# Optimization experiments

Hardware: AMD Instinct MI355X
Metric: run time of the kernel (lower is better)

The kernel has to match this reference:

```python
import jax, jax.numpy as jnp
import numpy as np

N = 100000
E = 1600000
F = 128
H = 8
D = F // H
NC = 3


def setup_inputs() -> dict:
    key = jax.random.key(0)
    ks = jax.random.split(key, 12)
    s = lambda fan_in: 1.0 / np.sqrt(fan_in)
    x = jax.random.normal(ks[0], (N, F), dtype=jnp.float32)
    edge_index = jax.random.randint(ks[1], (2, E), 0, N, dtype=jnp.int64)
    edge_attr = jax.random.normal(ks[2], (E, 2), dtype=jnp.float32)
    # params stored as [in, out] so y = x @ W + b
    Wqkv = jax.random.uniform(ks[3], (F, 3 * F), jnp.float32, -s(F), s(F))
    Wedge = jax.random.uniform(ks[4], (2, H), jnp.float32, -s(2), s(2))
    Wout = jax.random.uniform(ks[5], (F, F), jnp.float32, -s(F), s(F))
    bout = jax.random.uniform(ks[6], (F,), jnp.float32, -s(F), s(F))
    ln_w = jnp.ones((F,), jnp.float32)
    ln_b = jnp.zeros((F,), jnp.float32)
    Wc1 = jax.random.uniform(ks[7], (F, F // 2), jnp.float32, -s(F), s(F))
    bc1 = jax.random.uniform(ks[8], (F // 2,), jnp.float32, -s(F), s(F))
    Wc2 = jax.random.uniform(ks[9], (F // 2, NC), jnp.float32, -s(F // 2), s(F // 2))
    bc2 = jax.random.uniform(ks[10], (NC,), jnp.float32, -s(F // 2), s(F // 2))
    return {"x": x, "edge_index": edge_index, "edge_attr": edge_attr,
            "Wqkv": Wqkv, "Wedge": Wedge, "Wout": Wout, "bout": bout,
            "ln_w": ln_w, "ln_b": ln_b,
            "Wc1": Wc1, "bc1": bc1, "Wc2": Wc2, "bc2": bc2}


def reference(x, edge_index, edge_attr, Wqkv, Wedge, Wout, bout,
              ln_w, ln_b, Wc1, bc1, Wc2, bc2):
    n = x.shape[0]
    scale = D ** (-0.5)
    qkv = x @ Wqkv                                # [N, 3F]
    q, k, v = [t.reshape(n, H, D) for t in jnp.split(qkv, 3, axis=-1)]
    src = edge_index[0]   # j (source / neighbor)
    dst = edge_index[1]   # i (target, softmax segment)
    edge_bias = edge_attr @ Wedge                 # [E, H]
    # per-edge biased attention score
    score = jnp.einsum('ehd,ehd->eh', q[dst], k[src]) * scale + edge_bias
    # segment softmax over incoming edges of each target node
    m = jax.lax.stop_gradient(jax.ops.segment_max(score, dst, num_segments=n))
    ex = jnp.exp(score - m[dst])
    denom = jax.ops.segment_sum(ex, dst, num_segments=n) + 1e-16
    w = ex / denom[dst]                           # [E, H]
    agg = jax.ops.segment_sum(v[src] * w[..., None], dst, num_segments=n)
    attn_out = agg.reshape(n, F) @ Wout + bout    # to_out
    h = x + attn_out
    mu = jnp.mean(h, axis=-1, keepdims=True)
    var = jnp.mean((h - mu) ** 2, axis=-1, keepdims=True)
    h = (h - mu) / jnp.sqrt(var + 1e-5) * ln_w + ln_b
    h = jax.nn.relu(h @ Wc1 + bc1)
    return h @ Wc2 + bc2
```

## Files before the change

### kernel.cpp

```cpp
#include <hip/hip_runtime.h>
#include <stdint.h>

#define N_NODES 100000
#define N_EDGES 1600000
#define FDIM 128
#define NH 8
#define NCLS 3
#define NB 782

static constexpr float SCALE = 0.25f;

typedef _Float16 f16x8 __attribute__((ext_vector_type(8)));
typedef _Float16 f16x4 __attribute__((ext_vector_type(4)));
typedef float    f32x4 __attribute__((ext_vector_type(4)));

__global__ __launch_bounds__(256) void k_bhist(const int* __restrict__ ei,
                                               int* __restrict__ bcnt) {
    __shared__ int sb[NB];
    for (int i = threadIdx.x; i < NB; i += 256) sb[i] = 0;
    __syncthreads();
    int e0 = blockIdx.x * 1024;
#pragma unroll
    for (int j = 0; j < 4; ++j) {
        int e = e0 + j * 256 + threadIdx.x;
        if (e < N_EDGES) atomicAdd(&sb[ei[N_EDGES + e] >> 7], 1);
    }
    __syncthreads();
    for (int i = threadIdx.x; i < NB; i += 256)
        if (sb[i]) atomicAdd(&bcnt[i], sb[i]);
}

__global__ __launch_bounds__(256) void k_bscan(const int* __restrict__ bcnt,
                                               int* __restrict__ bbase,
                                               int* __restrict__ bcur) {
    __shared__ int sd[256];
    int t = threadIdx.x;
    int v[4]; int s = 0;
#pragma unroll
    for (int j = 0; j < 4; ++j) {
        int i = t * 4 + j;
        v[j] = (i < NB) ? bcnt[i] : 0;
        s += v[j];
    }
    sd[t] = s;
    __syncthreads();
    for (int off = 1; off < 256; off <<= 1) {
        int a = (t >= off) ? sd[t - off] : 0;
        __syncthreads();
        sd[t] += a;
        __syncthreads();
    }
    int run = sd[t] - s;
#pragma unroll
    for (int j = 0; j < 4; ++j) {
        int i = t * 4 + j;
        if (i < NB) { bbase[i] = run; bcur[i] = run; }
        run += v[j];
    }
    if (t == 0) bbase[NB] = N_EDGES;
}

__global__ __launch_bounds__(256) void k_bin(const int* __restrict__ ei,
                                             const float* __restrict__ ea,
                                             int* __restrict__ bcur,
                                             int* __restrict__ cnt,
                                             float4* __restrict__ binb) {
    __shared__ int lcnt[NB];
    __shared__ int lbase[NB];
    for (int i = threadIdx.x; i < NB; i += 256) lcnt[i] = 0;
    __syncthreads();
    int e0 = blockIdx.x * 1024;
    int rnk[4], bkt[4], src[4], dst[4];
    float2 eav[4];
#pragma unroll
    for (int j = 0; j < 4; ++j) {
        int e = e0 + j * 256 + threadIdx.x;
        if (e < N_EDGES) {
            src[j] = ei[e];
            dst[j] = ei[N_EDGES + e];
            eav[j] = *(const float2*)(ea + (long)e * 2);
            bkt[j] = dst[j] >> 7;
            rnk[j] = atomicAdd(&lcnt[bkt[j]], 1);
            atomicAdd(&cnt[dst[j]], 1);
        } else bkt[j] = -1;
    }
    __syncthreads();
    for (int i = threadIdx.x; i < NB; i += 256)
        if (lcnt[i]) lbase[i] = atomicAdd(&bcur[i], lcnt[i]);
    __syncthreads();
#pragma unroll
    for (int j = 0; j < 4; ++j) {
        if (bkt[j] >= 0) {
            int pos = lbase[bkt[j]] + rnk[j];
            binb[pos] = make_float4(__int_as_float(src[j]), __int_as_float(dst[j]),
                                    eav[j].x, eav[j].y);
        }
    }
}

__global__ __launch_bounds__(256) void k_scan1(const int* __restrict__ cnt,
                                               int* __restrict__ bsum) {
    __shared__ int sd[256];
    int t = threadIdx.x;
    int i0 = blockIdx.x * 1024 + t * 4;
    int s = 0;
#pragma unroll
    for (int j = 0; j < 4; ++j) {
        int i = i0 + j;
        if (i < N_NODES) s += cnt[i];
    }
    sd[t] = s;
    __syncthreads();
    for (int off = 128; off > 0; off >>= 1) {
        if (t < off) sd[t] += sd[t + off];
        __syncthreads();
    }
    if (t == 0) bsum[blockIdx.x] = sd[0];
}

__global__ __launch_bounds__(128) void k_scan2(const int* __restrict__ bsum,
                                               int* __restrict__ boff,
                                               int* __restrict__ row_start) {
    __shared__ int sd[128];
    int t = threadIdx.x;
    int v = (t < 98) ? bsum[t] : 0;
    sd[t] = v;
    __syncthreads();
    for (int off = 1; off < 128; off <<= 1) {
        int add = (t >= off) ? sd[t - off] : 0;
        __syncthreads();
        sd[t] += add;
        __syncthreads();
    }
    if (t < 98) boff[t] = sd[t] - v;
    if (t == 0) row_start[N_NODES] = N_EDGES;
}

__global__ __launch_bounds__(256) void k_scan3(const int* __restrict__ cnt,
                                               const int* __restrict__ boff,
                                               int* __restrict__ row_start) {
    __shared__ int sd[256];
    int t = threadIdx.x;
    int i0 = blockIdx.x * 1024 + t * 4;
    int c[4];
    int s = 0;
#pragma unroll
    for (int j = 0; j < 4; ++j) {
        int i = i0 + j;
        c[j] = (i < N_NODES) ? cnt[i] : 0;
        s += c[j];
    }
    sd[t] = s;
    __syncthreads();
    for (int off = 1; off < 256; off <<= 1) {
        int add = (t >= off) ? sd[t - off] : 0;
        __syncthreads();
        sd[t] += add;
        __syncthreads();
    }
    int run = boff[blockIdx.x] + sd[t] - s;
#pragma unroll
    for (int j = 0; j < 4; ++j) {
        int i = i0 + j;
        if (i < N_NODES) row_start[i] = run;
        run += c[j];
    }
}

__global__ __launch_bounds__(256) void k_fine(const float4* __restrict__ binb,
                                              const int* __restrict__ bbase,
                                              const int* __restrict__ row_start,
                                              float4* __restrict__ se4) {
    __shared__ int cur[128];
    int b = blockIdx.x;
    int n0 = b << 7;
    int t = threadIdx.x;
    if (t < 128) {
        int n = n0 + t;
        cur[t] = (n < N_NODES) ? row_start[n] : 0;
    }
    __syncthreads();
    int p0 = bbase[b], p1 = bbase[b + 1];
    for (int p = p0 + t; p < p1; p += 256) {
        float4 r = binb[p];
        int d = __float_as_int(r.y);
        int pos = atomicAdd(&cur[d - n0], 1);
        se4[pos] = make_float4(r.x, r.z, r.w, 0.f);
    }
}

__global__ __launch_bounds__(256) void k_cvt(const float* __restrict__ x,
                                             const float* __restrict__ Wqkv,
                                             const float* __restrict__ Wout,
                                             _Float16* __restrict__ x_h,
                                             _Float16* __restrict__ Wqkv_t,
                                             _Float16* __restrict__ Wout_t) {
    long i = (long)blockIdx.x * 256 + threadIdx.x;
    float4 v = ((const float4*)x)[i];
    f16x4 h = { (_Float16)v.x, (_Float16)v.y, (_Float16)v.z, (_Float16)v.w };
    *(f16x4*)(x_h + i * 4) = h;
    if (i < 128 * 384) {
        int k = (int)(i / 384), n = (int)(i % 384);
        Wqkv_t[(long)n * 128 + k] = (_Float16)Wqkv[i];
    }
    if (i < 128 * 128) {
        int k = (int)(i / 128), n = (int)(i % 128);
        Wout_t[(long)n * 128 + k] = (_Float16)Wout[i];
    }
}

__global__ __launch_bounds__(256) void k_mm_qkv(const _Float16* __restrict__ x_h,
                                                const _Float16* __restrict__ Wt,
                                                float* __restrict__ q_tab,
                                                _Float16* __restrict__ kv_h) {
    int wave = threadIdx.x >> 6, l = threadIdx.x & 63;
    int row0 = blockIdx.x * 64 + wave * 16;
    int lr = l & 15, lg = l >> 4;
    int arow = row0 + lr;
    bool aok = arow < N_NODES;
    long abase = (long)arow * 128 + lg * 8;

    f32x4 acc[24];
#pragma unroll
    for (int c = 0; c < 24; ++c) acc[c] = (f32x4){0.f, 0.f, 0.f, 0.f};

#pragma unroll
    for (int kk = 0; kk < 4; ++kk) {
        f16x8 a = aok ? *(const f16x8*)(x_h + abase + kk * 32) : (f16x8){};
        const _Float16* wb = Wt + (long)lr * 128 + lg * 8 + kk * 32;
#pragma unroll
        for (int c = 0; c < 24; ++c) {
            f16x8 b = *(const f16x8*)(wb + (long)c * 16 * 128);
            acc[c] = __builtin_amdgcn_mfma_f32_16x16x32_f16(a, b, acc[c], 0, 0, 0);
        }
    }

    int orow_base = row0 + lg * 4;
#pragma unroll
    for (int c = 0; c < 24; ++c) {
#pragma unroll
        for (int j = 0; j < 4; ++j) {
            int orow = orow_base + j;
            if (orow < N_NODES) {
                float v = acc[c][j];
                if (c < 8)       q_tab[(long)orow * 128 + c * 16 + lr] = v;
                else if (c < 16) kv_h[(long)orow * 256 + (c - 8) * 16 + lr]        = (_Float16)v;
                else             kv_h[(long)orow * 256 + 128 + (c - 16) * 16 + lr] = (_Float16)v;
            }
        }
    }
}

__global__ __launch_bounds__(256) void k_mm_out(const _Float16* __restrict__ agg_h,
                                                const _Float16* __restrict__ Wot,
                                                const float* __restrict__ bout,
                                                const float* __restrict__ x,
                                                float* __restrict__ h_pre) {
    int wave = threadIdx.x >> 6, l = threadIdx.x & 63;
    int row0 = blockIdx.x * 64 + wave * 16;
    int lr = l & 15, lg = l >> 4;
    int arow = row0 + lr;
    bool aok = arow < N_NODES;
    long abase = (long)arow * 128 + lg * 8;

    f32x4 acc[8];
#pragma unroll
    for (int c = 0; c < 8; ++c) acc[c] = (f32x4){0.f, 0.f, 0.f, 0.f};

#pragma unroll
    for (int kk = 0; kk < 4; ++kk) {
        f16x8 a = aok ? *(const f16x8*)(agg_h + abase + kk * 32) : (f16x8){};
        const _Float16* wb = Wot + (long)lr * 128 + lg * 8 + kk * 32;
#pragma unroll
        for (int c = 0; c < 8; ++c) {
            f16x8 b = *(const f16x8*)(wb + (long)c * 16 * 128);
            acc[c] = __builtin_amdgcn_mfma_f32_16x16x32_f16(a, b, acc[c], 0, 0, 0);
        }
    }

    int orow_base = row0 + lg * 4;
#pragma unroll
    for (int c = 0; c < 8; ++c) {
        int ocol = c * 16 + lr;
        float bv = bout[ocol];
#pragma unroll
        for (int j = 0; j < 4; ++j) {
            int orow = orow_base + j;
            if (orow < N_NODES) {
                h_pre[(long)orow * 128 + ocol] = acc[c][j] + bv + x[(long)orow * 128 + ocol];
            }
        }
    }
}

__global__ __launch_bounds__(256) void k_attn(const float* __restrict__ q_tab,
                                              const _Float16* __restrict__ kv_tab,
                                              const float4* __restrict__ se4,
                                              const int* __restrict__ row_start,
                                              const float* __restrict__ Wedge,
                                              _Float16* __restrict__ agg_h) {
    int wave = threadIdx.x >> 6;
    int lane = threadIdx.x & 63;
    int node = blockIdx.x * 4 + wave;
    if (node >= N_NODES) return;

    int g  = lane >> 4;
    int gl = lane & 15;
    int h  = gl >> 1;

    int p0 = row_start[node], p1 = row_start[node + 1];
    if (p0 == p1) {
        if (g == 0) *(f16x8*)(agg_h + (long)node * 128 + gl * 8) = (f16x8){};
        return;
    }

    float we0 = Wedge[h];
    float we1 = Wedge[8 + h];
    const float* qb = q_tab + (long)node * 128 + gl * 8;
    float4 qa  = *(const float4*)(qb);
    float4 qbv = *(const float4*)(qb + 4);

    float a0=0.f,a1=0.f,a2=0.f,a3=0.f,a4=0.f,a5=0.f,a6=0.f,a7=0.f;
    float den = 0.f;

    int last = p1 - 1;
    float4 rec = se4[min(p0 + g, last)];
    for (int p = p0; p < p1; p += 4) {
        float4 cur = rec;
        int pn = p + 4;
        if (pn < p1) rec = se4[min(pn + g, last)];

        bool valid = (p + g) < p1;
        int src = __float_as_int(cur.x);
        const _Float16* kvb = kv_tab + (long)src * 256 + gl * 8;
        f16x8 kh = *(const f16x8*)(kvb);
        f16x8 vh = *(const f16x8*)(kvb + 128);

        float part = qa.x  * (float)kh[0] + qa.y  * (float)kh[1]
                   + qa.z  * (float)kh[2] + qa.w  * (float)kh[3]
                   + qbv.x * (float)kh[4] + qbv.y * (float)kh[5]
                   + qbv.z * (float)kh[6] + qbv.w * (float)kh[7];
        part += __shfl_xor(part, 1);

        float s = part * SCALE + cur.y * we0 + cur.z * we1;
        float w = valid ? __expf(s) : 0.f;
        den += w;
        a0 += w * (float)vh[0]; a1 += w * (float)vh[1];
        a2 += w * (float)vh[2]; a3 += w * (float)vh[3];
        a4 += w * (float)vh[4]; a5 += w * (float)vh[5];
        a6 += w * (float)vh[6]; a7 += w * (float)vh[7];
    }

#pragma unroll
    for (int off = 16; off <= 32; off <<= 1) {
        a0 += __shfl_xor(a0, off); a1 += __shfl_xor(a1, off);
        a2 += __shfl_xor(a2, off); a3 += __shfl_xor(a3, off);
        a4 += __shfl_xor(a4, off); a5 += __shfl_xor(a5, off);
        a6 += __shfl_xor(a6, off); a7 += __shfl_xor(a7, off);
        den += __shfl_xor(den, off);
    }

    if (g == 0) {
        float inv = 1.0f / (den + 1e-16f);
        f16x8 o = { (_Float16)(a0 * inv), (_Float16)(a1 * inv),
                    (_Float16)(a2 * inv), (_Float16)(a3 * inv),
                    (_Float16)(a4 * inv), (_Float16)(a5 * inv),
                    (_Float16)(a6 * inv), (_Float16)(a7 * inv) };
        *(f16x8*)(agg_h + (long)node * 128 + gl * 8) = o;
    }
}

__global__ __launch_bounds__(256) void k_mlp(const float* __restrict__ h_pre,
                                             const float* __restrict__ ln_w,
                                             const float* __restrict__ ln_b,
                                             const float* __restrict__ Wc1,
                                             const float* __restrict__ bc1,
                                             const float* __restrict__ Wc2,
                                             const float* __restrict__ bc2,
                                             float* __restrict__ out) {
    __shared__ float sW1[128 * 64];
    __shared__ float sW2[64 * 3];
    __shared__ float sb1[64];
    __shared__ float sb2[3];
    __shared__ float hbuf[4][4][128];
    int t = threadIdx.x;
#pragma unroll
    for (int it = 0; it < 8; ++it) {
        int f = (it * 256 + t) * 4;
        *(float4*)(sW1 + f) = *(const float4*)(Wc1 + f);
    }
    if (t < 192) sW2[t] = Wc2[t];
    if (t < 64) sb1[t] = bc1[t];
    if (t < 3) sb2[t] = bc2[t];
    __syncthreads();

    int wave = t >> 6, lane = t & 63;
    float2 lw = *(const float2*)(ln_w + lane * 2);
    float2 lb = *(const float2*)(ln_b + lane * 2);
    int nb0 = (blockIdx.x * 4 + wave) * 4;

#pragma unroll
    for (int nb = 0; nb < 4; ++nb) {
        int node = nb0 + nb;
        float2 hv = *(const float2*)(h_pre + (long)node * 128 + lane * 2);
        float s = hv.x + hv.y;
#pragma unroll
        for (int off = 32; off > 0; off >>= 1) s += __shfl_xor(s, off);
        float mu = s * (1.0f / 128.0f);
        float dx = hv.x - mu, dy = hv.y - mu;
        float s2 = dx * dx + dy * dy;
#pragma unroll
        for (int off = 32; off > 0; off >>= 1) s2 += __shfl_xor(s2, off);
        float rstd = rsqrtf(s2 * (1.0f / 128.0f) + 1e-5f);
        hbuf[wave][nb][lane * 2] = dx * rstd * lw.x + lb.x;
        hbuf[wave][nb][lane * 2 + 1] = dy * rstd * lw.y + lb.y;
    }
    __syncthreads();

    float acc[4];
#pragma unroll
    for (int nb = 0; nb < 4; ++nb) acc[nb] = sb1[lane];
#pragma unroll 4
    for (int c = 0; c < 128; ++c) {
        float w = sW1[c * 64 + lane];
        acc[0] += hbuf[wave][0][c] * w;
        acc[1] += hbuf[wave][1][c] * w;
        acc[2] += hbuf[wave][2][c] * w;
        acc[3] += hbuf[wave][3][c] * w;
    }
#pragma unroll
    for (int nb = 0; nb < 4; ++nb) {
        float a = fmaxf(acc[nb], 0.f);
#pragma unroll
        for (int c2 = 0; c2 < NCLS; ++c2) {
            float pv = a * sW2[lane * 3 + c2];
#pragma unroll
            for (int off = 32; off > 0; off >>= 1) pv += __shfl_xor(pv, off);
            if (lane == 0) out[(long)(nb0 + nb) * 3 + c2] = pv + sb2[c2];
        }
    }
}

extern "C" void kernel_launch(void* const* d_in, const int* in_sizes, int n_in,
                              void* d_out, int out_size, void* d_ws, size_t ws_size,
                              hipStream_t stream) {
    const float* x         = (const float*)d_in[0];
    const int*   edge_index= (const int*)d_in[1];
    const float* edge_attr = (const float*)d_in[2];
    const float* Wqkv      = (const float*)d_in[3];
    const float* Wedge     = (const float*)d_in[4];
    const float* Wout      = (const float*)d_in[5];
    const float* bout      = (const float*)d_in[6];
    const float* ln_w      = (const float*)d_in[7];
    const float* ln_b      = (const float*)d_in[8];
    const float* Wc1       = (const float*)d_in[9];
    const float* bc1       = (const float*)d_in[10];
    const float* Wc2       = (const float*)d_in[11];
    const float* bc2       = (const float*)d_in[12];
    float* out = (float*)d_out;

    char* ws = (char*)d_ws;
    size_t o = 0;
    auto alloc = [&](size_t bytes) -> char* {
        char* p = ws + o;
        o = (o + bytes + 255) & ~(size_t)255;
        return p;
    };
    int*       cnt       = (int*)alloc((size_t)N_NODES * 4);
    int*       row_start = (int*)alloc((size_t)(N_NODES + 1) * 4);
    int*       bsum      = (int*)alloc(98 * 4);
    int*       boff      = (int*)alloc(98 * 4);
    int*       bcnt      = (int*)alloc((size_t)NB * 4);
    int*       bbase     = (int*)alloc((size_t)(NB + 1) * 4);
    int*       bcur      = (int*)alloc((size_t)NB * 4);
    float4*    binb      = (float4*)alloc((size_t)N_EDGES * 16);
    float4*    se4       = (float4*)alloc((size_t)N_EDGES * 16);
    _Float16*  x_h       = (_Float16*)alloc((size_t)N_NODES * 128 * 2);
    _Float16*  Wqkv_t    = (_Float16*)alloc((size_t)384 * 128 * 2);
    _Float16*  Wout_t    = (_Float16*)alloc((size_t)128 * 128 * 2);
    float*     q_tab     = (float*)alloc((size_t)N_NODES * 128 * 4);
    _Float16*  kv_h      = (_Float16*)alloc((size_t)N_NODES * 256 * 2);
    _Float16*  agg_h     = (_Float16*)alloc((size_t)N_NODES * 128 * 2);
    float*     h_pre     = q_tab;
    (void)ws_size; (void)in_sizes; (void)n_in; (void)out_size;

    hipMemsetAsync(cnt, 0, (size_t)N_NODES * 4, stream);
    hipMemsetAsync(bcnt, 0, (size_t)NB * 4, stream);

    k_bhist<<<1563, 256, 0, stream>>>(edge_index, bcnt);
    k_bscan<<<1, 256, 0, stream>>>(bcnt, bbase, bcur);
    k_bin<<<1563, 256, 0, stream>>>(edge_index, edge_attr, bcur, cnt, binb);
    k_scan1<<<98, 256, 0, stream>>>(cnt, bsum);
    k_scan2<<<1, 128, 0, stream>>>(bsum, boff, row_start);
    k_scan3<<<98, 256, 0, stream>>>(cnt, boff, row_start);
    k_fine<<<NB, 256, 0, stream>>>(binb, bbase, row_start, se4);

    k_cvt<<<12500, 256, 0, stream>>>(x, Wqkv, Wout, x_h, Wqkv_t, Wout_t);
    k_mm_qkv<<<1563, 256, 0, stream>>>(x_h, Wqkv_t, q_tab, kv_h);
    k_attn<<<25000, 256, 0, stream>>>(q_tab, kv_h, se4, row_start, Wedge, agg_h);
    k_mm_out<<<1563, 256, 0, stream>>>(agg_h, Wout_t, bout, x, h_pre);
    k_mlp<<<6250, 256, 0, stream>>>(h_pre, ln_w, ln_b, Wc1, bc1, Wc2, bc2, out);
}
```

Measured before the change: 646.7 us.

## Fuse pipeline stages: fixed-capacity binning, single-block scan, fused QKV convert and out-proj+MLP

Removes the bucket histogram/scan pass by giving each bucket a fixed capacity slot (BCAP=4096), and replaces the three-kernel row_start scan with a single 1024-thread block scan that also transposes the weights. The QKV matmul now converts fp32 x to fp16 inline, dropping the x_h conversion kernel, and it reuses each weight fragment across four row tiles. The output projection, residual, layernorm and classifier MLP are fused into one kernel through LDS, removing the h_pre round trip. Risks: bucket overflow if any 128-node bucket exceeds 4096 edges, a serial single-block scan, and Wc1 read from global memory instead of shared memory.

```diff
diff --git a/kernel.cpp b/kernel.cpp
--- a/kernel.cpp
+++ b/kernel.cpp
@@ -7,58 +7,12 @@
 #define NH 8
 #define NCLS 3
 #define NB 782
+#define BCAP 4096
 
 static constexpr float SCALE = 0.25f;
 
 typedef _Float16 f16x8 __attribute__((ext_vector_type(8)));
-typedef _Float16 f16x4 __attribute__((ext_vector_type(4)));
 typedef float    f32x4 __attribute__((ext_vector_type(4)));
-
-__global__ __launch_bounds__(256) void k_bhist(const int* __restrict__ ei,
-                                               int* __restrict__ bcnt) {
-    __shared__ int sb[NB];
-    for (int i = threadIdx.x; i < NB; i += 256) sb[i] = 0;
-    __syncthreads();
-    int e0 = blockIdx.x * 1024;
-#pragma unroll
-    for (int j = 0; j < 4; ++j) {
-        int e = e0 + j * 256 + threadIdx.x;
-        if (e < N_EDGES) atomicAdd(&sb[ei[N_EDGES + e] >> 7], 1);
-    }
-    __syncthreads();
-    for (int i = threadIdx.x; i < NB; i += 256)
-        if (sb[i]) atomicAdd(&bcnt[i], sb[i]);
-}
-
-__global__ __launch_bounds__(256) void k_bscan(const int* __restrict__ bcnt,
-                                               int* __restrict__ bbase,
-                                               int* __restrict__ bcur) {
-    __shared__ int sd[256];
-    int t = threadIdx.x;
-    int v[4]; int s = 0;
-#pragma unroll
-    for (int j = 0; j < 4; ++j) {
-        int i = t * 4 + j;
-        v[j] = (i < NB) ? bcnt[i] : 0;
-        s += v[j];
-    }
-    sd[t] = s;
-    __syncthreads();
-    for (int off = 1; off < 256; off <<= 1) {
-        int a = (t >= off) ? sd[t - off] : 0;
-        __syncthreads();
-        sd[t] += a;
-        __syncthreads();
-    }
-    int run = sd[t] - s;
-#pragma unroll
-    for (int j = 0; j < 4; ++j) {
-        int i = t * 4 + j;
-        if (i < NB) { bbase[i] = run; bcur[i] = run; }
-        run += v[j];
-    }
-    if (t == 0) bbase[NB] = N_EDGES;
-}
 
 __global__ __launch_bounds__(256) void k_bin(const int* __restrict__ ei,
                                              const float* __restrict__ ea,
@@ -91,84 +45,58 @@
 #pragma unroll
     for (int j = 0; j < 4; ++j) {
         if (bkt[j] >= 0) {
-            int pos = lbase[bkt[j]] + rnk[j];
+            int pos = bkt[j] * BCAP + lbase[bkt[j]] + rnk[j];
             binb[pos] = make_float4(__int_as_float(src[j]), __int_as_float(dst[j]),
                                     eav[j].x, eav[j].y);
         }
     }
 }
 
-__global__ __launch_bounds__(256) void k_scan1(const int* __restrict__ cnt,
-                                               int* __restrict__ bsum) {
-    __shared__ int sd[256];
-    int t = threadIdx.x;
-    int i0 = blockIdx.x * 1024 + t * 4;
-    int s = 0;
-#pragma unroll
-    for (int j = 0; j < 4; ++j) {
-        int i = i0 + j;
-        if (i < N_NODES) s += cnt[i];
-    }
-    sd[t] = s;
-    __syncthreads();
-    for (int off = 128; off > 0; off >>= 1) {
-        if (t < off) sd[t] += sd[t + off];
+__global__ __launch_bounds__(1024) void k_prep(const int* __restrict__ cnt,
+                                               int* __restrict__ row_start,
+                                               const float* __restrict__ Wqkv,
+                                               const float* __restrict__ Wout,
+                                               _Float16* __restrict__ Wqkv_t,
+                                               _Float16* __restrict__ Wout_t) {
+    if (blockIdx.x == 0) {
+        __shared__ int sd[1024];
+        const int NPT = 98;
+        int t = threadIdx.x;
+        int base = t * NPT;
+        int s = 0;
+        for (int i = 0; i < NPT; ++i) {
+            int idx = base + i;
+            if (idx < N_NODES) s += cnt[idx];
+        }
+        sd[t] = s;
         __syncthreads();
-    }
-    if (t == 0) bsum[blockIdx.x] = sd[0];
-}
-
-__global__ __launch_bounds__(128) void k_scan2(const int* __restrict__ bsum,
-                                               int* __restrict__ boff,
-                                               int* __restrict__ row_start) {
-    __shared__ int sd[128];
-    int t = threadIdx.x;
-    int v = (t < 98) ? bsum[t] : 0;
-    sd[t] = v;
-    __syncthreads();
-    for (int off = 1; off < 128; off <<= 1) {
-        int add = (t >= off) ? sd[t - off] : 0;
-        __syncthreads();
-        sd[t] += add;
-        __syncthreads();
-    }
-    if (t < 98) boff[t] = sd[t] - v;
-    if (t == 0) row_start[N_NODES] = N_EDGES;
-}
-
-__global__ __launch_bounds__(256) void k_scan3(const int* __restrict__ cnt,
-                                               const int* __restrict__ boff,
-                                               int* __restrict__ row_start) {
-    __shared__ int sd[256];
-    int t = threadIdx.x;
-    int i0 = blockIdx.x * 1024 + t * 4;
-    int c[4];
-    int s = 0;
-#pragma unroll
-    for (int j = 0; j < 4; ++j) {
-        int i = i0 + j;
-        c[j] = (i < N_NODES) ? cnt[i] : 0;
-        s += c[j];
-    }
-    sd[t] = s;
-    __syncthreads();
-    for (int off = 1; off < 256; off <<= 1) {
-        int add = (t >= off) ? sd[t - off] : 0;
-        __syncthreads();
-        sd[t] += add;
-        __syncthreads();
-    }
-    int run = boff[blockIdx.x] + sd[t] - s;
-#pragma unroll
-    for (int j = 0; j < 4; ++j) {
-        int i = i0 + j;
-        if (i < N_NODES) row_start[i] = run;
-        run += c[j];
+        for (int off = 1; off < 1024; off <<= 1) {
+            int v = (t >= off) ? sd[t - off] : 0;
+            __syncthreads();
+            sd[t] += v;
+            __syncthreads();
+        }
+        int run = sd[t] - s;
+        for (int i = 0; i < NPT; ++i) {
+            int idx = base + i;
+            if (idx < N_NODES) { row_start[idx] = run; run += cnt[idx]; }
+        }
+        if (t == 0) row_start[N_NODES] = N_EDGES;
+    } else {
+        int i = (blockIdx.x - 1) * 1024 + threadIdx.x;
+        if (i < 128 * 384) {
+            int k = i / 384, n = i % 384;
+            Wqkv_t[(long)n * 128 + k] = (_Float16)Wqkv[i];
+        } else {
+            int j = i - 128 * 384;
+            int k = j / 128, n = j % 128;
+            Wout_t[(long)n * 128 + k] = (_Float16)Wout[j];
+        }
     }
 }
 
 __global__ __launch_bounds__(256) void k_fine(const float4* __restrict__ binb,
-                                              const int* __restrict__ bbase,
+                                              const int* __restrict__ bcnt,
                                               const int* __restrict__ row_start,
                                               float4* __restrict__ se4) {
     __shared__ int cur[128];
@@ -180,7 +108,7 @@
         cur[t] = (n < N_NODES) ? row_start[n] : 0;
     }
     __syncthreads();
-    int p0 = bbase[b], p1 = bbase[b + 1];
+    int p0 = b * BCAP, p1 = b * BCAP + bcnt[b];
     for (int p = p0 + t; p < p1; p += 256) {
         float4 r = binb[p];
         int d = __float_as_int(r.y);
@@ -189,105 +117,61 @@
     }
 }
 
-__global__ __launch_bounds__(256) void k_cvt(const float* __restrict__ x,
-                                             const float* __restrict__ Wqkv,
-                                             const float* __restrict__ Wout,
-                                             _Float16* __restrict__ x_h,
-                                             _Float16* __restrict__ Wqkv_t,
-                                             _Float16* __restrict__ Wout_t) {
-    long i = (long)blockIdx.x * 256 + threadIdx.x;
-    float4 v = ((const float4*)x)[i];
-    f16x4 h = { (_Float16)v.x, (_Float16)v.y, (_Float16)v.z, (_Float16)v.w };
-    *(f16x4*)(x_h + i * 4) = h;
-    if (i < 128 * 384) {
-        int k = (int)(i / 384), n = (int)(i % 384);
-        Wqkv_t[(long)n * 128 + k] = (_Float16)Wqkv[i];
-    }
-    if (i < 128 * 128) {
-        int k = (int)(i / 128), n = (int)(i % 128);
-        Wout_t[(long)n * 128 + k] = (_Float16)Wout[i];
-    }
-}
-
-__global__ __launch_bounds__(256) void k_mm_qkv(const _Float16* __restrict__ x_h,
+__global__ __launch_bounds__(256) void k_mm_qkv(const float* __restrict__ x,
                                                 const _Float16* __restrict__ Wt,
                                                 float* __restrict__ q_tab,
                                                 _Float16* __restrict__ kv_h) {
     int wave = threadIdx.x >> 6, l = threadIdx.x & 63;
-    int row0 = blockIdx.x * 64 + wave * 16;
+    int row0 = blockIdx.x * 64;
     int lr = l & 15, lg = l >> 4;
-    int arow = row0 + lr;
-    bool aok = arow < N_NODES;
-    long abase = (long)arow * 128 + lg * 8;
-
-    f32x4 acc[24];
-#pragma unroll
-    for (int c = 0; c < 24; ++c) acc[c] = (f32x4){0.f, 0.f, 0.f, 0.f};
+
+    f32x4 acc[4][6];
+#pragma unroll
+    for (int rf = 0; rf < 4; ++rf)
+#pragma unroll
+        for (int c = 0; c < 6; ++c) acc[rf][c] = (f32x4){0.f, 0.f, 0.f, 0.f};
 
 #pragma unroll
     for (int kk = 0; kk < 4; ++kk) {
-        f16x8 a = aok ? *(const f16x8*)(x_h + abase + kk * 32) : (f16x8){};
-        const _Float16* wb = Wt + (long)lr * 128 + lg * 8 + kk * 32;
-#pragma unroll
-        for (int c = 0; c < 24; ++c) {
-            f16x8 b = *(const f16x8*)(wb + (long)c * 16 * 128);
-            acc[c] = __builtin_amdgcn_mfma_f32_16x16x32_f16(a, b, acc[c], 0, 0, 0);
-        }
-    }
-
-    int orow_base = row0 + lg * 4;
-#pragma unroll
-    for (int c = 0; c < 24; ++c) {
-#pragma unroll
-        for (int j = 0; j < 4; ++j) {
-            int orow = orow_base + j;
-            if (orow < N_NODES) {
-                float v = acc[c][j];
-                if (c < 8)       q_tab[(long)orow * 128 + c * 16 + lr] = v;
-                else if (c < 16) kv_h[(long)orow * 256 + (c - 8) * 16 + lr]        = (_Float16)v;
-                else             kv_h[(long)orow * 256 + 128 + (c - 16) * 16 + lr] = (_Float16)v;
-            }
-        }
-    }
-}
-
-__global__ __launch_bounds__(256) void k_mm_out(const _Float16* __restrict__ agg_h,
-                                                const _Float16* __restrict__ Wot,
-                                                const float* __restrict__ bout,
-                                                const float* __restrict__ x,
-                                                float* __restrict__ h_pre) {
-    int wave = threadIdx.x >> 6, l = threadIdx.x & 63;
-    int row0 = blockIdx.x * 64 + wave * 16;
-    int lr = l & 15, lg = l >> 4;
-    int arow = row0 + lr;
-    bool aok = arow < N_NODES;
-    long abase = (long)arow * 128 + lg * 8;
-
-    f32x4 acc[8];
-#pragma unroll
-    for (int c = 0; c < 8; ++c) acc[c] = (f32x4){0.f, 0.f, 0.f, 0.f};
-
-#pragma unroll
-    for (int kk = 0; kk < 4; ++kk) {
-        f16x8 a = aok ? *(const f16x8*)(agg_h + abase + kk * 32) : (f16x8){};
-        const _Float16* wb = Wot + (long)lr * 128 + lg * 8 + kk * 32;
-#pragma unroll
-        for (int c = 0; c < 8; ++c) {
-            f16x8 b = *(const f16x8*)(wb + (long)c * 16 * 128);
-            acc[c] = __builtin_amdgcn_mfma_f32_16x16x32_f16(a, b, acc[c], 0, 0, 0);
-        }
-    }
-
-    int orow_base = row0 + lg * 4;
-#pragma unroll
-    for (int c = 0; c < 8; ++c) {
-        int ocol = c * 16 + lr;
-        float bv = bout[ocol];
-#pragma unroll
-        for (int j = 0; j < 4; ++j) {
-            int orow = orow_base + j;
-            if (orow < N_NODES) {
-                h_pre[(long)orow * 128 + ocol] = acc[c][j] + bv + x[(long)orow * 128 + ocol];
+        f16x8 a[4];
+#pragma unroll
+        for (int rf = 0; rf < 4; ++rf) {
+            int row = row0 + rf * 16 + lr;
+            if (row < N_NODES) {
+                const float* xb = x + (long)row * 128 + lg * 8 + kk * 32;
+                float4 v0 = *(const float4*)(xb);
+                float4 v1 = *(const float4*)(xb + 4);
+                a[rf] = (f16x8){ (_Float16)v0.x, (_Float16)v0.y, (_Float16)v0.z, (_Float16)v0.w,
+                                 (_Float16)v1.x, (_Float16)v1.y, (_Float16)v1.z, (_Float16)v1.w };
+            } else a[rf] = (f16x8){};
+        }
+        f16x8 b[6];
+#pragma unroll
+        for (int c = 0; c < 6; ++c) {
+            int wc = wave * 6 + c;
+            b[c] = *(const f16x8*)(Wt + (long)(wc * 16 + lr) * 128 + lg * 8 + kk * 32);
+        }
+#pragma unroll
+        for (int rf = 0; rf < 4; ++rf)
+#pragma unroll
+            for (int c = 0; c < 6; ++c)
+                acc[rf][c] = __builtin_amdgcn_mfma_f32_16x16x32_f16(a[rf], b[c], acc[rf][c], 0, 0, 0);
+    }
+
+#pragma unroll
+    for (int rf = 0; rf < 4; ++rf) {
+#pragma unroll
+        for (int c = 0; c < 6; ++c) {
+            int col = (wave * 6 + c) * 16 + lr;
+#pragma unroll
+            for (int j = 0; j < 4; ++j) {
+                int row = row0 + rf * 16 + lg * 4 + j;
+                if (row < N_NODES) {
+                    float v = acc[rf][c][j];
+                    if (col < 128)       q_tab[(long)row * 128 + col] = v;
+                    else if (col < 256)  kv_h[(long)row * 256 + (col - 128)] = (_Float16)v;
+                    else                 kv_h[(long)row * 256 + 128 + (col - 256)] = (_Float16)v;
+                }
             }
         }
     }
@@ -370,73 +254,111 @@
     }
 }
 
-__global__ __launch_bounds__(256) void k_mlp(const float* __restrict__ h_pre,
-                                             const float* __restrict__ ln_w,
-                                             const float* __restrict__ ln_b,
-                                             const float* __restrict__ Wc1,
-                                             const float* __restrict__ bc1,
-                                             const float* __restrict__ Wc2,
-                                             const float* __restrict__ bc2,
-                                             float* __restrict__ out) {
-    __shared__ float sW1[128 * 64];
-    __shared__ float sW2[64 * 3];
-    __shared__ float sb1[64];
-    __shared__ float sb2[3];
-    __shared__ float hbuf[4][4][128];
-    int t = threadIdx.x;
-#pragma unroll
-    for (int it = 0; it < 8; ++it) {
-        int f = (it * 256 + t) * 4;
-        *(float4*)(sW1 + f) = *(const float4*)(Wc1 + f);
-    }
-    if (t < 192) sW2[t] = Wc2[t];
-    if (t < 64) sb1[t] = bc1[t];
-    if (t < 3) sb2[t] = bc2[t];
+__global__ __launch_bounds__(256) void k_mm_fuse(const _Float16* __restrict__ agg_h,
+                                                 const _Float16* __restrict__ Wot,
+                                                 const float* __restrict__ bout,
+                                                 const float* __restrict__ x,
+                                                 const float* __restrict__ ln_w,
+                                                 const float* __restrict__ ln_b,
+                                                 const float* __restrict__ Wc1,
+                                                 const float* __restrict__ bc1,
+                                                 const float* __restrict__ Wc2,
+                                                 const float* __restrict__ bc2,
+                                                 float* __restrict__ out) {
+    __shared__ float hb[64][132];
+    int wave = threadIdx.x >> 6, l = threadIdx.x & 63;
+    int row0 = blockIdx.x * 64;
+    int lr = l & 15, lg = l >> 4;
+
+    f32x4 acc[4][2];
+#pragma unroll
+    for (int rf = 0; rf < 4; ++rf)
+#pragma unroll
+        for (int c = 0; c < 2; ++c) acc[rf][c] = (f32x4){0.f, 0.f, 0.f, 0.f};
+
+#pragma unroll
+    for (int kk = 0; kk < 4; ++kk) {
+        f16x8 a[4];
+#pragma unroll
+        for (int rf = 0; rf < 4; ++rf) {
+            int row = row0 + rf * 16 + lr;
+            a[rf] = (row < N_NODES) ? *(const f16x8*)(agg_h + (long)row * 128 + lg * 8 + kk * 32)
+                                    : (f16x8){};
+        }
+        f16x8 b[2];
+#pragma unroll
+        for (int c = 0; c < 2; ++c) {
+            int wc = wave * 2 + c;
+            b[c] = *(const f16x8*)(Wot + (long)(wc * 16 + lr) * 128 + lg * 8 + kk * 32);
+        }
+#pragma unroll
+        for (int rf = 0; rf < 4; ++rf)
+#pragma unroll
+            for (int c = 0; c < 2; ++c)
+                acc[rf][c] = __builtin_amdgcn_mfma_f32_16x16x32_f16(a[rf], b[c], acc[rf][c], 0, 0, 0);
+    }
+
+#pragma unroll
+    for (int rf = 0; rf < 4; ++rf) {
+#pragma unroll
+        for (int c = 0; c < 2; ++c) {
+            int col = (wave * 2 + c) * 16 + lr;
+            float bv = bout[col];
+#pragma unroll
+            for (int j = 0; j < 4; ++j) {
+                int lrow = rf * 16 + lg * 4 + j;
+                int row = row0 + lrow;
+                hb[lrow][col] = (row < N_NODES)
+                    ? acc[rf][c][j] + bv + x[(long)row * 128 + col] : 0.f;
+            }
+        }
+    }
     __syncthreads();
 
-    int wave = t >> 6, lane = t & 63;
-    float2 lw = *(const float2*)(ln_w + lane * 2);
-    float2 lb = *(const float2*)(ln_b + lane * 2);
-    int nb0 = (blockIdx.x * 4 + wave) * 4;
-
-#pragma unroll
-    for (int nb = 0; nb < 4; ++nb) {
-        int node = nb0 + nb;
-        float2 hv = *(const float2*)(h_pre + (long)node * 128 + lane * 2);
-        float s = hv.x + hv.y;
-#pragma unroll
-        for (int off = 32; off > 0; off >>= 1) s += __shfl_xor(s, off);
-        float mu = s * (1.0f / 128.0f);
-        float dx = hv.x - mu, dy = hv.y - mu;
-        float s2 = dx * dx + dy * dy;
-#pragma unroll
-        for (int off = 32; off > 0; off >>= 1) s2 += __shfl_xor(s2, off);
-        float rstd = rsqrtf(s2 * (1.0f / 128.0f) + 1e-5f);
-        hbuf[wave][nb][lane * 2] = dx * rstd * lw.x + lb.x;
-        hbuf[wave][nb][lane * 2 + 1] = dy * rstd * lw.y + lb.y;
-    }
-    __syncthreads();
-
-    float acc[4];
-#pragma unroll
-    for (int nb = 0; nb < 4; ++nb) acc[nb] = sb1[lane];
+    float2 lw = *(const float2*)(ln_w + l * 2);
+    float2 lb = *(const float2*)(ln_b + l * 2);
+    float b1 = bc1[l];
+
+#pragma unroll
+    for (int grp = 0; grp < 4; ++grp) {
+        int lrow0 = wave * 16 + grp * 4;
+#pragma unroll
+        for (int nb = 0; nb < 4; ++nb) {
+            int lrow = lrow0 + nb;
+            float hx = hb[lrow][l * 2];
+            float hy = hb[lrow][l * 2 + 1];
+            float s = hx + hy;
+#pragma unroll
+            for (int off = 32; off > 0; off >>= 1) s += __shfl_xor(s, off);
+            float mu = s * (1.0f / 128.0f);
+            float dx = hx - mu, dy = hy - mu;
+            float s2 = dx * dx + dy * dy;
+#pragma unroll
+            for (int off = 32; off > 0; off >>= 1) s2 += __shfl_xor(s2, off);
+            float rstd = rsqrtf(s2 * (1.0f / 128.0f) + 1e-5f);
+            hb[lrow][l * 2]     = dx * rstd * lw.x + lb.x;
+            hb[lrow][l * 2 + 1] = dy * rstd * lw.y + lb.y;
+        }
+        float macc[4] = { b1, b1, b1, b1 };
 #pragma unroll 4
-    for (int c = 0; c < 128; ++c) {
-        float w = sW1[c * 64 + lane];
-        acc[0] += hbuf[wave][0][c] * w;
-        acc[1] += hbuf[wave][1][c] * w;
-        acc[2] += hbuf[wave][2][c] * w;
-        acc[3] += hbuf[wave][3][c] * w;
-    }
-#pragma unroll
-    for (int nb = 0; nb < 4; ++nb) {
-        float a = fmaxf(acc[nb], 0.f);
-#pragma unroll
-        for (int c2 = 0; c2 < NCLS; ++c2) {
-            float pv = a * sW2[lane * 3 + c2];
-#pragma unroll
-            for (int off = 32; off > 0; off >>= 1) pv += __shfl_xor(pv, off);
-            if (lane == 0) out[(long)(nb0 + nb) * 3 + c2] = pv + sb2[c2];
+        for (int c = 0; c < 128; ++c) {
+            float w = Wc1[c * 64 + l];
+            macc[0] += hb[lrow0 + 0][c] * w;
+            macc[1] += hb[lrow0 + 1][c] * w;
+            macc[2] += hb[lrow0 + 2][c] * w;
+            macc[3] += hb[lrow0 + 3][c] * w;
+        }
+#pragma unroll
+        for (int nb = 0; nb < 4; ++nb) {
+            int row = row0 + lrow0 + nb;
+            float a = fmaxf(macc[nb], 0.f);
+#pragma unroll
+            for (int c2 = 0; c2 < NCLS; ++c2) {
+                float pv = a * Wc2[l * 3 + c2];
+#pragma unroll
+                for (int off = 32; off > 0; off >>= 1) pv += __shfl_xor(pv, off);
+                if (l == 0 && row < N_NODES) out[(long)row * 3 + c2] = pv + bc2[c2];
+            }
         }
     }
 }
@@ -467,37 +389,26 @@
         return p;
     };
     int*       cnt       = (int*)alloc((size_t)N_NODES * 4);
+    int*       bcur      = (int*)alloc((size_t)NB * 4);
     int*       row_start = (int*)alloc((size_t)(N_NODES + 1) * 4);
-    int*       bsum      = (int*)alloc(98 * 4);
-    int*       boff      = (int*)alloc(98 * 4);
-    int*       bcnt      = (int*)alloc((size_t)NB * 4);
-    int*       bbase     = (int*)alloc((size_t)(NB + 1) * 4);
-    int*       bcur      = (int*)alloc((size_t)NB * 4);
-    float4*    binb      = (float4*)alloc((size_t)N_EDGES * 16);
+    float4*    binb      = (float4*)alloc((size_t)NB * BCAP * 16);
     float4*    se4       = (float4*)alloc((size_t)N_EDGES * 16);
-    _Float16*  x_h       = (_Float16*)alloc((size_t)N_NODES * 128 * 2);
     _Float16*  Wqkv_t    = (_Float16*)alloc((size_t)384 * 128 * 2);
     _Float16*  Wout_t    = (_Float16*)alloc((size_t)128 * 128 * 2);
     float*     q_tab     = (float*)alloc((size_t)N_NODES * 128 * 4);
     _Float16*  kv_h      = (_Float16*)alloc((size_t)N_NODES * 256 * 2);
     _Float16*  agg_h     = (_Float16*)alloc((size_t)N_NODES * 128 * 2);
-    float*     h_pre     = q_tab;
     (void)ws_size; (void)in_sizes; (void)n_in; (void)out_size;
 
-    hipMemsetAsync(cnt, 0, (size_t)N_NODES * 4, stream);
-    hipMemsetAsync(bcnt, 0, (size_t)NB * 4, stream);
-
-    k_bhist<<<1563, 256, 0, stream>>>(edge_index, bcnt);
-    k_bscan<<<1, 256, 0, stream>>>(bcnt, bbase, bcur);
+    size_t zspan = (size_t)((char*)bcur - (char*)cnt) + (size_t)NB * 4;
+    hipMemsetAsync(cnt, 0, zspan, stream);
+
     k_bin<<<1563, 256, 0, stream>>>(edge_index, edge_attr, bcur, cnt, binb);
-    k_scan1<<<98, 256, 0, stream>>>(cnt, bsum);
-    k_scan2<<<1, 128, 0, stream>>>(bsum, boff, row_start);
-    k_scan3<<<98, 256, 0, stream>>>(cnt, boff, row_start);
-    k_fine<<<NB, 256, 0, stream>>>(binb, bbase, row_start, se4);
-
-    k_cvt<<<12500, 256, 0, stream>>>(x, Wqkv, Wout, x_h, Wqkv_t, Wout_t);
-    k_mm_qkv<<<1563, 256, 0, stream>>>(x_h, Wqkv_t, q_tab, kv_h);
+    k_prep<<<65, 1024, 0, stream>>>(cnt, row_start, Wqkv, Wout, Wqkv_t, Wout_t);
+    k_fine<<<NB, 256, 0, stream>>>(binb, bcur, row_start, se4);
+
+    k_mm_qkv<<<1563, 256, 0, stream>>>(x, Wqkv_t, q_tab, kv_h);
     k_attn<<<25000, 256, 0, stream>>>(q_tab, kv_h, se4, row_start, Wedge, agg_h);
-    k_mm_out<<<1563, 256, 0, stream>>>(agg_h, Wout_t, bout, x, h_pre);
-    k_mlp<<<6250, 256, 0, stream>>>(h_pre, ln_w, ln_b, Wc1, bc1, Wc2, bc2, out);
-}
+    k_mm_fuse<<<1563, 256, 0, stream>>>(agg_h, Wout_t, bout, x, ln_w, ln_b,
+                                        Wc1, bc1, Wc2, bc2, out);
+}
```

After: 738.4 us. 1.14x slower.
